# Kernel tuning notes

Hardware: AMD Instinct MI355X
Metric: run time of the kernel (lower is better)

The kernel has to match this reference:

```python
import jax, jax.numpy as jnp
import numpy as np

B = 131072
COUNT = 8
L1, L2, L3 = 512, 16, 32


def setup_inputs() -> dict:
    key = jax.random.key(0)
    ks = jax.random.split(key, 10)
    return {
        "accum": jax.random.normal(ks[0], (B, 2 * (L1 + COUNT)), dtype=jnp.float32),
        "us": jax.random.uniform(ks[1], (B,), dtype=jnp.float32),
        "l1_w": jax.random.normal(ks[2], (L2 * COUNT, 2 * L1), dtype=jnp.float32) * 0.02,
        "l1_b": jax.random.normal(ks[3], (L2 * COUNT,), dtype=jnp.float32) * 0.02,
        "l2_w": jax.random.normal(ks[4], (L3 * COUNT, L2), dtype=jnp.float32) * 0.05,
        "l2_b": jax.random.normal(ks[5], (L3 * COUNT,), dtype=jnp.float32) * 0.05,
        "out_w": jax.random.normal(ks[6], (COUNT, L3), dtype=jnp.float32) * 0.05,
        "out_b": jax.random.normal(ks[7], (COUNT,), dtype=jnp.float32) * 0.05,
        "psqt_indices": jax.random.randint(ks[8], (B,), 0, COUNT),
        "layer_stack_indices": jax.random.randint(ks[9], (B,), 0, COUNT),
    }


def reference(accum, us, l1_w, l1_b, l2_w, l2_b, out_w, out_b,
              psqt_indices, layer_stack_indices):
    n = accum.shape[0]
    rows = jnp.arange(n)
    lsi = layer_stack_indices.astype(jnp.int32)

    # split accumulator: [w_main(512), w_psqt(8), b_main(512), b_psqt(8)]
    w_main = accum[:, :L1]
    w_psqt = accum[:, L1:L1 + COUNT]
    b_main = accum[:, L1 + COUNT:2 * L1 + COUNT]
    b_psqt = accum[:, 2 * L1 + COUNT:]
    main_accum = jnp.concatenate([w_main, b_main], axis=1)  # [B, 1024]

    # LayerStacks: dense compute over all stacks, then per-sample gather
    l1s = (main_accum @ l1_w.T + l1_b).reshape(n, COUNT, L2)
    l1y = jnp.clip(l1s[rows, lsi], 0.0, 1.0)                # [B, L2]
    l2s = (l1y @ l2_w.T + l2_b).reshape(n, COUNT, L3)
    l2y = jnp.clip(l2s[rows, lsi], 0.0, 1.0)                # [B, L3]
    l3s = (l2y @ out_w.T + out_b)                           # [B, COUNT]
    net_out = l3s[rows, lsi][:, None]                       # [B, 1]

    # psqt combine
    pi = psqt_indices.astype(jnp.int32)[:, None]
    wpsqt = jnp.take_along_axis(w_psqt, pi, axis=1)
    bpsqt = jnp.take_along_axis(b_psqt, pi, axis=1)
    us_ = us.reshape(-1, 1)
    return net_out + (wpsqt - bpsqt) * (us_ - 0.5)
```

## Files before the change

### kernel.cpp

```cpp
#include <hip/hip_runtime.h>
#include <hip/hip_bf16.h>

#define NCOUNT 8
#define B_TOTAL 131072
#define W_WIN 1024
#define BLK 256

typedef __attribute__((ext_vector_type(8))) short bf16x8;
typedef __attribute__((ext_vector_type(4))) float f32x4;
typedef __attribute__((ext_vector_type(16))) float f32x16;

__device__ inline short bf_cvt(float x) {
    __hip_bfloat16 h = __float2bfloat16(x);
    return *reinterpret_cast<short*>(&h);
}
__device__ inline bf16x8 cvt8(float4 a, float4 b) {
    bf16x8 r;
    r[0] = bf_cvt(a.x); r[1] = bf_cvt(a.y); r[2] = bf_cvt(a.z); r[3] = bf_cvt(a.w);
    r[4] = bf_cvt(b.x); r[5] = bf_cvt(b.y); r[6] = bf_cvt(b.z); r[7] = bf_cvt(b.w);
    return r;
}

__device__ inline void wg_barrier_lgkm() {
    asm volatile("s_waitcnt lgkmcnt(0)" ::: "memory");
    __builtin_amdgcn_s_barrier();
    asm volatile("" ::: "memory");
}

__device__ inline int atx(int row, int kbf) {
    return (row * 1024 + kbf) ^ ((row & 7) << 3);
}

__global__ __launch_bounds__(BLK, 2) void nnue_mfma_kernel(
    const float* __restrict__ accum,
    const float* __restrict__ us,
    const float* __restrict__ l1_w,
    const float* __restrict__ l1_b,
    const float* __restrict__ l2_w,
    const float* __restrict__ l2_b,
    const float* __restrict__ out_w,
    const float* __restrict__ out_b,
    const int*   __restrict__ psqt_indices,
    const int*   __restrict__ lsi,
    float*       __restrict__ out)
{
    __shared__ unsigned short list[W_WIN];
    __shared__ int cnt;
    __shared__ __align__(16) short At[32 * 1024];
    __shared__ __align__(16) float psq[2][32][16];
    __shared__ __align__(16) f32x4 l1part[2][3][64];
    __shared__ __align__(16) float l1y[2][16 * 20];
    __shared__ float epiw[64];

    const int l    = blockIdx.y;
    const int base = blockIdx.x * W_WIN;
    const int tid  = threadIdx.x;
    const int lane = tid & 63;
    const int wid  = tid >> 6;

    if (tid == 0) cnt = 0;
    __syncthreads();
    for (int i = tid; i < W_WIN; i += BLK)
        if (lsi[base + i] == l) list[atomicAdd(&cnt, 1)] = (unsigned short)i;
    if (tid < 64)
        epiw[tid] = (tid < 32) ? l2_b[l * 32 + tid] : out_w[l * 32 + (tid - 32)];
    __syncthreads();
    const int n = cnt;
    if (n == 0) return;

    const int jlow  = lane & 15;
    const int g     = lane >> 4;
    const int col32 = lane & 31;
    const int h     = lane >> 5;

    const float* wrow = l1_w + (((size_t)l * 16 + jlow) << 10);
    bf16x8 wfrag[8];
    #pragma unroll
    for (int i = 0; i < 8; ++i) {
        const int kf = (wid * 8 + i) * 32 + g * 8;
        wfrag[i] = cvt8(*(const float4*)(wrow + kf), *(const float4*)(wrow + kf + 4));
    }
    const float* w2row = l2_w + ((size_t)l * 32 + col32) * 16 + h * 8;
    const bf16x8 w2frag = cvt8(*(const float4*)(w2row), *(const float4*)(w2row + 4));
    const float l1bias = l1_b[l * 16 + jlow];
    const float outb   = out_b[l];

    const int srow  = tid >> 5;
    const int scol8 = tid & 31;
    const int pr    = tid >> 2;
    const int ppart = tid & 3;
    const int psf   = (ppart < 2) ? (512 + 4 * ppart) : (1032 + 4 * (ppart - 2));

    float4 pfa[16], pfb[16], pfq;
    float usn = 0.f, usc; int pin = 0, pic;

    auto issue_pf = [&](int tbn) {
        #pragma unroll
        for (int rr = 0; rr < 4; ++rr) {
            const int mi = tbn + 8 * rr + srow;
            const int s  = base + list[mi < n ? mi : n - 1];
            const float* src = accum + (size_t)s * 1040;
            #pragma unroll
            for (int p = 0; p < 4; ++p) {
                const int sf = 8 * (scol8 + 32 * p) + (p >= 2 ? 8 : 0);
                pfa[rr * 4 + p] = *(const float4*)(src + sf);
                pfb[rr * 4 + p] = *(const float4*)(src + sf + 4);
            }
        }
        if (tid < 128) {
            const int mi = tbn + pr;
            const float* src = accum + (size_t)(base + list[mi < n ? mi : n - 1]) * 1040;
            pfq = *(const float4*)(src + psf);
        }
        if (lane < 16 && wid < 2) {
            const int mi = tbn + wid * 16 + jlow;
            const int s  = base + list[mi < n ? mi : n - 1];
            usn = us[s];
            pin = psqt_indices[s];
        }
    };

    auto stage = [&](int par) {
        #pragma unroll
        for (int rr = 0; rr < 4; ++rr) {
            const int row = 8 * rr + srow;
            #pragma unroll
            for (int p = 0; p < 4; ++p)
                *(bf16x8*)&At[atx(row, 8 * (scol8 + 32 * p))] =
                    cvt8(pfa[rr * 4 + p], pfb[rr * 4 + p]);
        }
        if (tid < 128) *(float4*)&psq[par][pr][ppart * 4] = pfq;
    };

    issue_pf(0);

    int par = 0;
    for (int tb = 0; tb < n; tb += 32, par ^= 1) {
        stage(par);
        wg_barrier_lgkm();
        usc = usn; pic = pin;
        if (tb + 32 < n) issue_pf(tb + 32);

        f32x4 a0 = {0.f, 0.f, 0.f, 0.f};
        f32x4 a1 = {0.f, 0.f, 0.f, 0.f};
        #pragma unroll
        for (int i = 0; i < 8; ++i) {
            const int kf = (wid * 8 + i) * 32 + g * 8;
            bf16x8 f0 = *(const bf16x8*)&At[atx(jlow,      kf)];
            bf16x8 f1 = *(const bf16x8*)&At[atx(jlow + 16, kf)];
            a0 = __builtin_amdgcn_mfma_f32_16x16x32_bf16(f0, wfrag[i], a0, 0, 0, 0);
            a1 = __builtin_amdgcn_mfma_f32_16x16x32_bf16(f1, wfrag[i], a1, 0, 0, 0);
        }
        if (wid != 0) l1part[0][wid - 1][lane] = a0;
        if (wid != 1) l1part[1][wid == 0 ? 0 : wid - 1][lane] = a1;
        wg_barrier_lgkm();

        if (wid < 2) {
            const int grp = wid;
            const f32x4 own = (wid == 0) ? a0 : a1;
            const f32x4 t0 = l1part[grp][0][lane];
            const f32x4 t1 = l1part[grp][1][lane];
            const f32x4 t2 = l1part[grp][2][lane];
            float* ly = l1y[grp];
            #pragma unroll
            for (int r = 0; r < 4; ++r) {
                float v = fminf(fmaxf(own[r] + t0[r] + t1[r] + t2[r] + l1bias, 0.f), 1.f);
                ly[(g * 4 + r) * 20 + jlow] = v;
            }
            __builtin_amdgcn_wave_barrier();
            asm volatile("s_waitcnt lgkmcnt(0)" ::: "memory");

            const float* lyr = ly + (col32 & 15) * 20 + h * 8;
            float4 y0 = *(const float4*)(lyr);
            float4 y1 = *(const float4*)(lyr + 4);
            const bf16x8 b2frag = cvt8(y0, y1);

            f32x16 acc2 = {};
            acc2 = __builtin_amdgcn_mfma_f32_32x32x16_bf16(w2frag, b2frag, acc2, 0, 0, 0);

            float partial = 0.f;
            #pragma unroll
            for (int r = 0; r < 16; ++r) {
                const int j2 = (r & 3) + 8 * (r >> 2) + 4 * h;
                float v = fminf(fmaxf(acc2[r] + epiw[j2], 0.f), 1.f);
                partial += v * epiw[32 + j2];
            }
            partial += __shfl_xor(partial, 32);

            const int mi = tb + grp * 16 + jlow;
            if (lane < 16 && mi < n) {
                const int s = base + list[mi];
                const float wp = psq[par][grp * 16 + jlow][pic];
                const float bp = psq[par][grp * 16 + jlow][8 + pic];
                out[s] = partial + outb + (wp - bp) * (usc - 0.5f);
            }
        }
    }
}

extern "C" void kernel_launch(void* const* d_in, const int* in_sizes, int n_in,
                              void* d_out, int out_size, void* d_ws, size_t ws_size,
                              hipStream_t stream) {
    const float* accum = (const float*)d_in[0];
    const float* us    = (const float*)d_in[1];
    const float* l1_w  = (const float*)d_in[2];
    const float* l1_b  = (const float*)d_in[3];
    const float* l2_w  = (const float*)d_in[4];
    const float* l2_b  = (const float*)d_in[5];
    const float* out_w = (const float*)d_in[6];
    const float* out_b = (const float*)d_in[7];
    const int*   psqt  = (const int*)d_in[8];
    const int*   lsi   = (const int*)d_in[9];
    float* out = (float*)d_out;

    dim3 grid(B_TOTAL / W_WIN, NCOUNT);
    nnue_mfma_kernel<<<grid, BLK, 0, stream>>>(
        accum, us, l1_w, l1_b, l2_w, l2_b, out_w, out_b, psqt, lsi, out);
}
```

Before: 109.5 us.

## Halve per-iteration row tile to 16 to raise occupancy to three blocks

Each loop iteration now processes 16 gathered samples instead of 32. This halves the shared At tile, the prefetch registers and the epilogue buffers, and drops the second MFMA accumulator and the second epilogue wave. Launch bounds are raised to 3 blocks per CU to use the freed LDS and registers for more latency hiding on the gathered loads. In exchange there are twice as many barrier-separated iterations per block, only one wave does the epilogue, and each weight fragment is reused across fewer rows.

```diff
diff --git a/kernel.cpp b/kernel.cpp
--- a/kernel.cpp
+++ b/kernel.cpp
@@ -31,7 +31,7 @@
     return (row * 1024 + kbf) ^ ((row & 7) << 3);
 }
 
-__global__ __launch_bounds__(BLK, 2) void nnue_mfma_kernel(
+__global__ __launch_bounds__(BLK, 3) void nnue_mfma_kernel(
     const float* __restrict__ accum,
     const float* __restrict__ us,
     const float* __restrict__ l1_w,
@@ -46,10 +46,10 @@
 {
     __shared__ unsigned short list[W_WIN];
     __shared__ int cnt;
-    __shared__ __align__(16) short At[32 * 1024];
-    __shared__ __align__(16) float psq[2][32][16];
-    __shared__ __align__(16) f32x4 l1part[2][3][64];
-    __shared__ __align__(16) float l1y[2][16 * 20];
+    __shared__ __align__(16) short At[16 * 1024];
+    __shared__ __align__(16) float psq[2][16][16];
+    __shared__ __align__(16) f32x4 l1part[3][64];
+    __shared__ __align__(16) float l1y[16 * 20];
     __shared__ float epiw[64];
 
     const int l    = blockIdx.y;
@@ -91,12 +91,12 @@
     const int ppart = tid & 3;
     const int psf   = (ppart < 2) ? (512 + 4 * ppart) : (1032 + 4 * (ppart - 2));
 
-    float4 pfa[16], pfb[16], pfq;
+    float4 pfa[8], pfb[8], pfq;
     float usn = 0.f, usc; int pin = 0, pic;
 
     auto issue_pf = [&](int tbn) {
         #pragma unroll
-        for (int rr = 0; rr < 4; ++rr) {
+        for (int rr = 0; rr < 2; ++rr) {
             const int mi = tbn + 8 * rr + srow;
             const int s  = base + list[mi < n ? mi : n - 1];
             const float* src = accum + (size_t)s * 1040;
@@ -107,13 +107,13 @@
                 pfb[rr * 4 + p] = *(const float4*)(src + sf + 4);
             }
         }
-        if (tid < 128) {
+        if (tid < 64) {
             const int mi = tbn + pr;
             const float* src = accum + (size_t)(base + list[mi < n ? mi : n - 1]) * 1040;
             pfq = *(const float4*)(src + psf);
         }
-        if (lane < 16 && wid < 2) {
-            const int mi = tbn + wid * 16 + jlow;
+        if (wid == 0 && lane < 16) {
+            const int mi = tbn + jlow;
             const int s  = base + list[mi < n ? mi : n - 1];
             usn = us[s];
             pin = psqt_indices[s];
@@ -122,55 +122,48 @@
 
     auto stage = [&](int par) {
         #pragma unroll
-        for (int rr = 0; rr < 4; ++rr) {
+        for (int rr = 0; rr < 2; ++rr) {
             const int row = 8 * rr + srow;
             #pragma unroll
             for (int p = 0; p < 4; ++p)
                 *(bf16x8*)&At[atx(row, 8 * (scol8 + 32 * p))] =
                     cvt8(pfa[rr * 4 + p], pfb[rr * 4 + p]);
         }
-        if (tid < 128) *(float4*)&psq[par][pr][ppart * 4] = pfq;
+        if (tid < 64) *(float4*)&psq[par][pr][ppart * 4] = pfq;
     };
 
     issue_pf(0);
 
     int par = 0;
-    for (int tb = 0; tb < n; tb += 32, par ^= 1) {
+    for (int tb = 0; tb < n; tb += 16, par ^= 1) {
         stage(par);
         wg_barrier_lgkm();
         usc = usn; pic = pin;
-        if (tb + 32 < n) issue_pf(tb + 32);
+        if (tb + 16 < n) issue_pf(tb + 16);
 
         f32x4 a0 = {0.f, 0.f, 0.f, 0.f};
-        f32x4 a1 = {0.f, 0.f, 0.f, 0.f};
         #pragma unroll
         for (int i = 0; i < 8; ++i) {
             const int kf = (wid * 8 + i) * 32 + g * 8;
-            bf16x8 f0 = *(const bf16x8*)&At[atx(jlow,      kf)];
-            bf16x8 f1 = *(const bf16x8*)&At[atx(jlow + 16, kf)];
+            bf16x8 f0 = *(const bf16x8*)&At[atx(jlow, kf)];
             a0 = __builtin_amdgcn_mfma_f32_16x16x32_bf16(f0, wfrag[i], a0, 0, 0, 0);
-            a1 = __builtin_amdgcn_mfma_f32_16x16x32_bf16(f1, wfrag[i], a1, 0, 0, 0);
-        }
-        if (wid != 0) l1part[0][wid - 1][lane] = a0;
-        if (wid != 1) l1part[1][wid == 0 ? 0 : wid - 1][lane] = a1;
+        }
+        if (wid != 0) l1part[wid - 1][lane] = a0;
         wg_barrier_lgkm();
 
-        if (wid < 2) {
-            const int grp = wid;
-            const f32x4 own = (wid == 0) ? a0 : a1;
-            const f32x4 t0 = l1part[grp][0][lane];
-            const f32x4 t1 = l1part[grp][1][lane];
-            const f32x4 t2 = l1part[grp][2][lane];
-            float* ly = l1y[grp];
+        if (wid == 0) {
+            const f32x4 t0 = l1part[0][lane];
+            const f32x4 t1 = l1part[1][lane];
+            const f32x4 t2 = l1part[2][lane];
             #pragma unroll
             for (int r = 0; r < 4; ++r) {
-                float v = fminf(fmaxf(own[r] + t0[r] + t1[r] + t2[r] + l1bias, 0.f), 1.f);
-                ly[(g * 4 + r) * 20 + jlow] = v;
+                float v = fminf(fmaxf(a0[r] + t0[r] + t1[r] + t2[r] + l1bias, 0.f), 1.f);
+                l1y[(g * 4 + r) * 20 + jlow] = v;
             }
             __builtin_amdgcn_wave_barrier();
             asm volatile("s_waitcnt lgkmcnt(0)" ::: "memory");
 
-            const float* lyr = ly + (col32 & 15) * 20 + h * 8;
+            const float* lyr = l1y + (col32 & 15) * 20 + h * 8;
             float4 y0 = *(const float4*)(lyr);
             float4 y1 = *(const float4*)(lyr + 4);
             const bf16x8 b2frag = cvt8(y0, y1);
@@ -187,11 +180,11 @@
             }
             partial += __shfl_xor(partial, 32);
 
-            const int mi = tb + grp * 16 + jlow;
+            const int mi = tb + jlow;
             if (lane < 16 && mi < n) {
                 const int s = base + list[mi];
-                const float wp = psq[par][grp * 16 + jlow][pic];
-                const float bp = psq[par][grp * 16 + jlow][8 + pic];
+                const float wp = psq[par][jlow][pic];
+                const float bp = psq[par][jlow][8 + pic];
                 out[s] = partial + outb + (wp - bp) * (usc - 0.5f);
             }
         }
```

After: 136.6 us. 1.25x slower.
